# Performance work log

Hardware: AMD Instinct MI355X
Metric: run time of the kernel (lower is better)

Reference implementation:

```python
import jax, jax.numpy as jnp
import numpy as np

EMBED_DIM = 1024
N_HEADS = 16
HEAD_DIM = EMBED_DIM // N_HEADS
SEQ_LEN = 4096


def setup_inputs() -> dict:
    key = jax.random.key(0)
    k1, k2 = jax.random.split(key)
    x = jax.random.normal(k1, (SEQ_LEN, EMBED_DIM), dtype=jnp.float32)
    # Linear params (lecun-normal-ish scale)
    W_qkv = jax.random.normal(k2, (EMBED_DIM, 3 * EMBED_DIM), dtype=jnp.float32) / np.sqrt(EMBED_DIM)
    b_qkv = jnp.zeros((3 * EMBED_DIM,), dtype=jnp.float32)
    return {"x": x, "W_qkv": W_qkv, "b_qkv": b_qkv}


def reference(x, W_qkv, b_qkv):
    T = x.shape[0]
    # Fused QKV projection: [T, 3*E]
    qkv = x @ W_qkv + b_qkv
    q, k, v = jnp.split(qkv, 3, axis=-1)
    # [T, N, H]
    q = q.reshape(T, N_HEADS, HEAD_DIM)
    k = k.reshape(T, N_HEADS, HEAD_DIM)
    v = v.reshape(T, N_HEADS, HEAD_DIM)
    # Standard SDPA (module does NOT pass is_causal, so full attention)
    scale = 1.0 / np.sqrt(HEAD_DIM).astype(np.float32)
    logits = jnp.einsum("qnh,knh->nqk", q, k) * scale  # [N, T, T]
    attn = jax.nn.softmax(logits, axis=-1)
    y = jnp.einsum("nqk,knh->qnh", attn, v)  # [T, N, H]
    return y
```

## Files before the change

kernel.cpp:

```cpp
#include <hip/hip_runtime.h>

#define T_SEQ 4096
#define EMB   1024
#define NH    16
#define HD    64
#define N3    3072

#define SCL2 0.18033688011112042f

using u16 = unsigned short;
using u32 = unsigned int;
typedef __bf16 bf16x8 __attribute__((ext_vector_type(8)));
typedef float  f32x4  __attribute__((ext_vector_type(4)));
typedef float  f32x16 __attribute__((ext_vector_type(16)));
typedef u16    u16x4  __attribute__((ext_vector_type(4)));
typedef u16    u16x8  __attribute__((ext_vector_type(8)));

#if __has_builtin(__builtin_amdgcn_exp2f)
#define EXP2(x) __builtin_amdgcn_exp2f(x)
#else
#define EXP2(x) exp2f(x)
#endif

__device__ inline u16 f2bf(float f) {
    union { float f; unsigned u; } v; v.f = f;
    unsigned u = v.u;
    u += 0x7FFFu + ((u >> 16) & 1u);
    return (u16)(u >> 16);
}

__global__ void convert_x_kernel(const float* __restrict__ x, u16* __restrict__ xb) {
    int i = (blockIdx.x * 256 + threadIdx.x) * 8;
    float4 a = *(const float4*)(x + i);
    float4 b = *(const float4*)(x + i + 4);
    u16x8 o;
    o[0] = f2bf(a.x); o[1] = f2bf(a.y); o[2] = f2bf(a.z); o[3] = f2bf(a.w);
    o[4] = f2bf(b.x); o[5] = f2bf(b.y); o[6] = f2bf(b.z); o[7] = f2bf(b.w);
    *(u16x8*)(xb + i) = o;
}

__global__ void transpose_w_kernel(const float* __restrict__ W, u16* __restrict__ Wt) {
    __shared__ float tile[64][72];
    int n0 = blockIdx.x * 64, k0 = blockIdx.y * 64;
    float qs = (n0 < 1024) ? SCL2 : 1.0f;
    int t = threadIdx.x;
#pragma unroll
    for (int p = 0; p < 16; ++p) {
        int idx = p * 256 + t;
        int r = idx >> 6, c = idx & 63;
        tile[r][c] = W[(k0 + r) * N3 + n0 + c];
    }
    __syncthreads();
    int c2 = t >> 2;
    int kg = (t & 3) * 16;
    u16x8 o0, o1;
#pragma unroll
    for (int j = 0; j < 8; ++j) o0[j] = f2bf(tile[kg + j][c2] * qs);
#pragma unroll
    for (int j = 0; j < 8; ++j) o1[j] = f2bf(tile[kg + 8 + j][c2] * qs);
    u16* dst = Wt + (n0 + c2) * EMB + k0 + kg;
    *(u16x8*)dst = o0;
    *(u16x8*)(dst + 8) = o1;
}

__global__ __launch_bounds__(256) void gemm_qkv_kernel(const u16* __restrict__ xb,
                                                       const u16* __restrict__ Wt,
                                                       const float* __restrict__ bias,
                                                       u16* __restrict__ qkv,
                                                       u16* __restrict__ Vt) {
    __shared__ __align__(16) u16 Alds[2][128 * 64];
    __shared__ __align__(16) u16 Blds[2][128 * 64];
    int tid = threadIdx.x;
    int lane = tid & 63, wave = tid >> 6;
    int wm = wave >> 1, wn = wave & 1;
    int m0 = blockIdx.y * 128, n0 = blockIdx.x * 128;
    int lr = lane & 15, lg = lane >> 4;

    f32x4 acc[4][4] = {};

    int srow = tid >> 3;
    int cg = (tid & 7) << 3;
    int sg = (((tid & 7) ^ (srow & 7)) << 3);
    const u16* aBase = xb + (size_t)(m0 + srow) * EMB + cg;
    const u16* bBase = Wt + (size_t)(n0 + srow) * EMB + cg;
    int wIdx = srow * 64 + sg;

    u16x8 va[4], vb[4];
#pragma unroll
    for (int p = 0; p < 4; ++p) {
        va[p] = *(const u16x8*)(aBase + (size_t)(p * 32) * EMB);
        vb[p] = *(const u16x8*)(bBase + (size_t)(p * 32) * EMB);
    }

    for (int kt = 0; kt < 16; ++kt) {
        u16* Al = Alds[kt & 1];
        u16* Bl = Blds[kt & 1];
#pragma unroll
        for (int p = 0; p < 4; ++p) {
            *(u16x8*)&Al[wIdx + p * 32 * 64] = va[p];
            *(u16x8*)&Bl[wIdx + p * 32 * 64] = vb[p];
        }
        if (kt < 15) {
            int kbase = (kt + 1) * 64;
#pragma unroll
            for (int p = 0; p < 4; ++p) {
                va[p] = *(const u16x8*)(aBase + (size_t)(p * 32) * EMB + kbase);
                vb[p] = *(const u16x8*)(bBase + (size_t)(p * 32) * EMB + kbase);
            }
        }
        __syncthreads();
#pragma unroll
        for (int ks = 0; ks < 2; ++ks) {
            bf16x8 af[4], bf[4];
#pragma unroll
            for (int mi = 0; mi < 4; ++mi) {
                int row = wm * 64 + mi * 16 + lr;
                int rsg = ((ks * 4 + lg) ^ (row & 7)) << 3;
                af[mi] = *(const bf16x8*)&Al[row * 64 + rsg];
            }
#pragma unroll
            for (int ni = 0; ni < 4; ++ni) {
                int row = wn * 64 + ni * 16 + lr;
                int rsg = ((ks * 4 + lg) ^ (row & 7)) << 3;
                bf[ni] = *(const bf16x8*)&Bl[row * 64 + rsg];
            }
#pragma unroll
            for (int mi = 0; mi < 4; ++mi)
#pragma unroll
                for (int ni = 0; ni < 4; ++ni)
                    acc[mi][ni] = __builtin_amdgcn_mfma_f32_16x16x32_bf16(af[mi], bf[ni], acc[mi][ni], 0, 0, 0);
        }
    }
    if (n0 < 2048) {
#pragma unroll
        for (int ni = 0; ni < 4; ++ni) {
            int n = n0 + wn * 64 + ni * 16 + lr;
            float bv = bias[n];
            if (n < 1024) bv *= SCL2;
#pragma unroll
            for (int mi = 0; mi < 4; ++mi) {
                int mrow = m0 + wm * 64 + mi * 16 + lg * 4;
#pragma unroll
                for (int r = 0; r < 4; ++r)
                    qkv[(mrow + r) * N3 + n] = f2bf(acc[mi][ni][r] + bv);
            }
        }
    } else {
#pragma unroll
        for (int ni = 0; ni < 4; ++ni) {
            int n = n0 + wn * 64 + ni * 16 + lr;
            float bv = bias[n];
            int nc = n - 2048;
#pragma unroll
            for (int mi = 0; mi < 4; ++mi) {
                int mrow = m0 + wm * 64 + mi * 16 + lg * 4;
                u16x4 o;
#pragma unroll
                for (int r = 0; r < 4; ++r) o[r] = f2bf(acc[mi][ni][r] + bv);
                *(u16x4*)&Vt[(size_t)nc * T_SEQ + mrow] = o;
            }
        }
    }
}

__device__ inline u32 cvtpk(float lo, float hi) {
    u32 r;
    asm("v_cvt_pk_bf16_f32 %0, %1, %2" : "=v"(r) : "v"(lo), "v"(hi));
    return r;
}

__device__ inline bf16x8 mk8(u32 w0, u32 w1, u32 w2, u32 w3) {
    union { u32 w[4]; bf16x8 v; } u;
    u.w[0] = w0; u.w[1] = w1; u.w[2] = w2; u.w[3] = w3;
    return u.v;
}

__device__ inline void pack2(f32x16 p, int hi, bf16x8& fe, bf16x8& fo) {
    u32 a0 = cvtpk(p[0], p[1]),   a1 = cvtpk(p[2], p[3]);
    u32 a2 = cvtpk(p[4], p[5]),   a3 = cvtpk(p[6], p[7]);
    u32 b0 = cvtpk(p[8], p[9]),   b1 = cvtpk(p[10], p[11]);
    u32 b2 = cvtpk(p[12], p[13]), b3 = cvtpk(p[14], p[15]);
    u32 xa0 = (u32)__shfl_xor((int)a0, 32), xa1 = (u32)__shfl_xor((int)a1, 32);
    u32 xa2 = (u32)__shfl_xor((int)a2, 32), xa3 = (u32)__shfl_xor((int)a3, 32);
    u32 xb0 = (u32)__shfl_xor((int)b0, 32), xb1 = (u32)__shfl_xor((int)b1, 32);
    u32 xb2 = (u32)__shfl_xor((int)b2, 32), xb3 = (u32)__shfl_xor((int)b3, 32);
    fe = hi ? mk8(xa2, xa3, a2, a3) : mk8(a0, a1, xa0, xa1);
    fo = hi ? mk8(xb2, xb3, b2, b3) : mk8(b0, b1, xb0, xb1);
}

#define KVROW 72

__global__ __launch_bounds__(512, 2) void attn_kernel(const u16* __restrict__ qkv,
                                                      const u16* __restrict__ Vt,
                                                      float* __restrict__ out) {
    __shared__ __align__(16) char smem[69632];
    u16* K0 = (u16*)smem;
    u16* V0 = (u16*)(smem + 9216);
    u16* K1 = (u16*)(smem + 18432);
    u16* V1 = (u16*)(smem + 27648);

    int tid = threadIdx.x, lane = tid & 63, wave = tid >> 6;
    int ql = lane & 31, hi = lane >> 5;
    int bid = blockIdx.x;
    int idx = bid >> 3;
    int h = 2 * (bid & 7) + (idx >> 4);
    int q0 = (idx & 15) * 256;

    bf16x8 qf[4];
    {
        const u16* qp = qkv + (size_t)(q0 + wave * 32 + ql) * N3 + h * HD;
#pragma unroll
        for (int c = 0; c < 4; ++c)
            qf[c] = *(const bf16x8*)(qp + c * 16 + hi * 8);
    }

    bf16x8 ones;
    {
        union { u16x8 u; bf16x8 b; } uu;
#pragma unroll
        for (int j = 0; j < 8; ++j) uu.u[j] = 0x3F80;
        ones = uu.b;
    }

    f32x16 acc0 = {}, acc1 = {}, acc2 = {};

    int srow0 = tid >> 3, spg = tid & 7;
    const u16* kptr = qkv + EMB + h * HD;
    const u16* vptr = Vt + (size_t)(h * HD) * T_SEQ;
    int woff0 = srow0 * KVROW + spg * 8;

    u16x8 kst0 = *(const u16x8*)(kptr + (size_t)srow0 * N3 + spg * 8);
    u16x8 vst0 = *(const u16x8*)(vptr + (size_t)srow0 * T_SEQ + spg * 8);

    int koff = ql * KVROW + hi * 8;

    for (int t = 0; t < 64; ++t) {
        u16* Kl = (t & 1) ? K1 : K0;
        u16* Vl = (t & 1) ? V1 : V0;
        *(u16x8*)&Kl[woff0] = kst0;
        *(u16x8*)&Vl[woff0] = vst0;
        if (t < 63) {
            const u16* kb = kptr + (size_t)(t + 1) * 64 * N3;
            const u16* vb = vptr + (t + 1) * 64;
            kst0 = *(const u16x8*)(kb + (size_t)srow0 * N3 + spg * 8);
            vst0 = *(const u16x8*)(vb + (size_t)srow0 * T_SEQ + spg * 8);
        }
        __syncthreads();

        f32x16 s0 = {}, s1 = {};
#pragma unroll
        for (int c = 0; c < 4; ++c) {
            bf16x8 kf = *(const bf16x8*)&Kl[koff + c * 16];
            s0 = __builtin_amdgcn_mfma_f32_32x32x16_bf16(kf, qf[c], s0, 0, 0, 0);
        }
#pragma unroll
        for (int c = 0; c < 4; ++c) {
            bf16x8 kf = *(const bf16x8*)&Kl[koff + 32 * KVROW + c * 16];
            s1 = __builtin_amdgcn_mfma_f32_32x32x16_bf16(kf, qf[c], s1, 0, 0, 0);
        }

#pragma unroll
        for (int r = 0; r < 16; ++r) s0[r] = EXP2(s0[r]);
#pragma unroll
        for (int r = 0; r < 16; ++r) s1[r] = EXP2(s1[r]);

        bf16x8 pa0, pa1, pa2, pa3;
        pack2(s0, hi, pa0, pa1);
        pack2(s1, hi, pa2, pa3);

#pragma unroll
        for (int c = 0; c < 4; ++c) {
            bf16x8 pb = (c == 0) ? pa0 : (c == 1) ? pa1 : (c == 2) ? pa2 : pa3;
            bf16x8 vf0 = *(const bf16x8*)&Vl[koff + c * 16];
            acc0 = __builtin_amdgcn_mfma_f32_32x32x16_bf16(vf0, pb, acc0, 0, 0, 0);
            bf16x8 vf1 = *(const bf16x8*)&Vl[koff + 32 * KVROW + c * 16];
            acc1 = __builtin_amdgcn_mfma_f32_32x32x16_bf16(vf1, pb, acc1, 0, 0, 0);
            acc2 = __builtin_amdgcn_mfma_f32_32x32x16_bf16(ones, pb, acc2, 0, 0, 0);
        }
    }

    __syncthreads();

    float inv = 1.0f / acc2[0];
    float* ob = (float*)smem + wave * (32 * 68);
#pragma unroll
    for (int g = 0; g < 4; ++g) {
        f32x4 w0 = { acc0[4 * g] * inv, acc0[4 * g + 1] * inv, acc0[4 * g + 2] * inv, acc0[4 * g + 3] * inv };
        *(f32x4*)&ob[ql * 68 + 8 * g + 4 * hi] = w0;
        f32x4 w1 = { acc1[4 * g] * inv, acc1[4 * g + 1] * inv, acc1[4 * g + 2] * inv, acc1[4 * g + 3] * inv };
        *(f32x4*)&ob[ql * 68 + 32 + 8 * g + 4 * hi] = w1;
    }
    asm volatile("s_waitcnt lgkmcnt(0)" ::: "memory");
#pragma unroll
    for (int qq = 0; qq < 8; ++qq) {
        int q = qq * 4 + (lane >> 4);
        int d4 = (lane & 15) * 4;
        f32x4 v = *(const f32x4*)&ob[q * 68 + d4];
        *(f32x4*)&out[(size_t)(q0 + wave * 32 + q) * EMB + h * HD + d4] = v;
    }
}

extern "C" void kernel_launch(void* const* d_in, const int* in_sizes, int n_in,
                              void* d_out, int out_size, void* d_ws, size_t ws_size,
                              hipStream_t stream) {
    (void)in_sizes; (void)n_in; (void)out_size; (void)ws_size;
    const float* x = (const float*)d_in[0];
    const float* W = (const float*)d_in[1];
    const float* b = (const float*)d_in[2];
    float* out = (float*)d_out;

    u16* xb  = (u16*)d_ws;
    u16* Wt  = xb  + (size_t)T_SEQ * EMB;
    u16* qkv = Wt  + (size_t)N3 * EMB;
    u16* Vt  = qkv + (size_t)T_SEQ * N3;

    convert_x_kernel<<<(T_SEQ * EMB) / (256 * 8), 256, 0, stream>>>(x, xb);
    transpose_w_kernel<<<dim3(N3 / 64, EMB / 64), 256, 0, stream>>>(W, Wt);
    gemm_qkv_kernel<<<dim3(N3 / 128, T_SEQ / 128), 256, 0, stream>>>(xb, Wt, b, qkv, Vt);
    attn_kernel<<<256, 512, 0, stream>>>(qkv, Vt, out);
}
```

Before: 132.2 us.

## Split attention KV range across two blocks and add combine kernel

Each attention block now covers half of the key/value sequence, doubling the grid from 256 to 512 blocks so that more of the 256 CUs hold two resident blocks. Partial unnormalized outputs and row sums go to the output buffer and to scratch space that reuses the dead xb/Wt workspace. A new combine kernel adds the partials and normalizes them. Q and K are also written to separate contiguous buffers instead of the interleaved qkv layout. The cost is an extra kernel launch and extra fp32 global traffic for the partials. Skipping max-subtraction stays safe only because the two halves share the same implicit reference point.

```diff
diff --git a/kernel.cpp b/kernel.cpp
--- a/kernel.cpp
+++ b/kernel.cpp
@@ -66,7 +66,8 @@
 __global__ __launch_bounds__(256) void gemm_qkv_kernel(const u16* __restrict__ xb,
                                                        const u16* __restrict__ Wt,
                                                        const float* __restrict__ bias,
-                                                       u16* __restrict__ qkv,
+                                                       u16* __restrict__ Qp,
+                                                       u16* __restrict__ Kp,
                                                        u16* __restrict__ Vt) {
     __shared__ __align__(16) u16 Alds[2][128 * 64];
     __shared__ __align__(16) u16 Blds[2][128 * 64];
@@ -137,12 +138,14 @@
             int n = n0 + wn * 64 + ni * 16 + lr;
             float bv = bias[n];
             if (n < 1024) bv *= SCL2;
+            u16* pl = (n < 1024) ? Qp : Kp;
+            int nc = n & 1023;
 #pragma unroll
             for (int mi = 0; mi < 4; ++mi) {
                 int mrow = m0 + wm * 64 + mi * 16 + lg * 4;
 #pragma unroll
                 for (int r = 0; r < 4; ++r)
-                    qkv[(mrow + r) * N3 + n] = f2bf(acc[mi][ni][r] + bv);
+                    pl[(size_t)(mrow + r) * EMB + nc] = f2bf(acc[mi][ni][r] + bv);
             }
         }
     } else {
@@ -190,9 +193,14 @@
 
 #define KVROW 72
 
-__global__ __launch_bounds__(512, 2) void attn_kernel(const u16* __restrict__ qkv,
+__global__ __launch_bounds__(512, 2) void attn_kernel(const u16* __restrict__ Qp,
+                                                      const u16* __restrict__ Kp,
                                                       const u16* __restrict__ Vt,
-                                                      float* __restrict__ out) {
+                                                      float* __restrict__ out,
+                                                      float* __restrict__ pA,
+                                                      float* __restrict__ pB,
+                                                      float* __restrict__ l0,
+                                                      float* __restrict__ l1) {
     __shared__ __align__(16) char smem[69632];
     u16* K0 = (u16*)smem;
     u16* V0 = (u16*)(smem + 9216);
@@ -202,13 +210,15 @@
     int tid = threadIdx.x, lane = tid & 63, wave = tid >> 6;
     int ql = lane & 31, hi = lane >> 5;
     int bid = blockIdx.x;
-    int idx = bid >> 3;
-    int h = 2 * (bid & 7) + (idx >> 4);
+    int half = bid >> 8;
+    int rem = bid & 255;
+    int idx = rem >> 3;
+    int h = 2 * (rem & 7) + (idx >> 4);
     int q0 = (idx & 15) * 256;
 
     bf16x8 qf[4];
     {
-        const u16* qp = qkv + (size_t)(q0 + wave * 32 + ql) * N3 + h * HD;
+        const u16* qp = Qp + (size_t)(q0 + wave * 32 + ql) * EMB + h * HD;
 #pragma unroll
         for (int c = 0; c < 4; ++c)
             qf[c] = *(const bf16x8*)(qp + c * 16 + hi * 8);
@@ -225,24 +235,24 @@
     f32x16 acc0 = {}, acc1 = {}, acc2 = {};
 
     int srow0 = tid >> 3, spg = tid & 7;
-    const u16* kptr = qkv + EMB + h * HD;
-    const u16* vptr = Vt + (size_t)(h * HD) * T_SEQ;
+    const u16* kptr = Kp + (size_t)(half * 2048) * EMB + h * HD;
+    const u16* vptr = Vt + (size_t)(h * HD) * T_SEQ + half * 2048;
     int woff0 = srow0 * KVROW + spg * 8;
 
-    u16x8 kst0 = *(const u16x8*)(kptr + (size_t)srow0 * N3 + spg * 8);
+    u16x8 kst0 = *(const u16x8*)(kptr + (size_t)srow0 * EMB + spg * 8);
     u16x8 vst0 = *(const u16x8*)(vptr + (size_t)srow0 * T_SEQ + spg * 8);
 
     int koff = ql * KVROW + hi * 8;
 
-    for (int t = 0; t < 64; ++t) {
+    for (int t = 0; t < 32; ++t) {
         u16* Kl = (t & 1) ? K1 : K0;
         u16* Vl = (t & 1) ? V1 : V0;
         *(u16x8*)&Kl[woff0] = kst0;
         *(u16x8*)&Vl[woff0] = vst0;
-        if (t < 63) {
-            const u16* kb = kptr + (size_t)(t + 1) * 64 * N3;
+        if (t < 31) {
+            const u16* kb = kptr + (size_t)(t + 1) * 64 * EMB;
             const u16* vb = vptr + (t + 1) * 64;
-            kst0 = *(const u16x8*)(kb + (size_t)srow0 * N3 + spg * 8);
+            kst0 = *(const u16x8*)(kb + (size_t)srow0 * EMB + spg * 8);
             vst0 = *(const u16x8*)(vb + (size_t)srow0 * T_SEQ + spg * 8);
         }
         __syncthreads();
@@ -281,23 +291,58 @@
 
     __syncthreads();
 
-    float inv = 1.0f / acc2[0];
+    if (hi == 0) {
+        float* dl = half ? l1 : l0;
+        dl[h * T_SEQ + q0 + wave * 32 + ql] = acc2[0];
+    }
+
     float* ob = (float*)smem + wave * (32 * 68);
 #pragma unroll
     for (int g = 0; g < 4; ++g) {
-        f32x4 w0 = { acc0[4 * g] * inv, acc0[4 * g + 1] * inv, acc0[4 * g + 2] * inv, acc0[4 * g + 3] * inv };
+        f32x4 w0 = { acc0[4 * g], acc0[4 * g + 1], acc0[4 * g + 2], acc0[4 * g + 3] };
         *(f32x4*)&ob[ql * 68 + 8 * g + 4 * hi] = w0;
-        f32x4 w1 = { acc1[4 * g] * inv, acc1[4 * g + 1] * inv, acc1[4 * g + 2] * inv, acc1[4 * g + 3] * inv };
+        f32x4 w1 = { acc1[4 * g], acc1[4 * g + 1], acc1[4 * g + 2], acc1[4 * g + 3] };
         *(f32x4*)&ob[ql * 68 + 32 + 8 * g + 4 * hi] = w1;
     }
     asm volatile("s_waitcnt lgkmcnt(0)" ::: "memory");
-#pragma unroll
-    for (int qq = 0; qq < 8; ++qq) {
-        int q = qq * 4 + (lane >> 4);
-        int d4 = (lane & 15) * 4;
-        f32x4 v = *(const f32x4*)&ob[q * 68 + d4];
-        *(f32x4*)&out[(size_t)(q0 + wave * 32 + q) * EMB + h * HD + d4] = v;
-    }
+    if (half == 0) {
+#pragma unroll
+        for (int qq = 0; qq < 8; ++qq) {
+            int q = qq * 4 + (lane >> 4);
+            int d4 = (lane & 15) * 4;
+            f32x4 v = *(const f32x4*)&ob[q * 68 + d4];
+            *(f32x4*)&out[(size_t)(q0 + wave * 32 + q) * EMB + h * HD + d4] = v;
+        }
+    } else {
+        float* P1h = (h < 14) ? (pA + (size_t)h * (T_SEQ * HD))
+                              : (pB + (size_t)(h - 14) * (T_SEQ * HD));
+#pragma unroll
+        for (int qq = 0; qq < 8; ++qq) {
+            int q = qq * 4 + (lane >> 4);
+            int d4 = (lane & 15) * 4;
+            f32x4 v = *(const f32x4*)&ob[q * 68 + d4];
+            *(f32x4*)&P1h[(size_t)(q0 + wave * 32 + q) * HD + d4] = v;
+        }
+    }
+}
+
+__global__ void combine_kernel(float* __restrict__ out,
+                               const float* __restrict__ pA,
+                               const float* __restrict__ pB,
+                               const float* __restrict__ l0,
+                               const float* __restrict__ l1) {
+    size_t idx = ((size_t)blockIdx.x * 256 + threadIdx.x) * 4;
+    int q = (int)(idx >> 10);
+    int e = (int)(idx & 1023);
+    int h = e >> 6, d = e & 63;
+    const float* p1 = (h < 14) ? (pA + (size_t)h * (T_SEQ * HD))
+                               : (pB + (size_t)(h - 14) * (T_SEQ * HD));
+    f32x4 o = *(const f32x4*)&out[idx];
+    f32x4 p = *(const f32x4*)&p1[(size_t)q * HD + d];
+    float inv = 1.0f / (l0[h * T_SEQ + q] + l1[h * T_SEQ + q]);
+    f32x4 r = { (o[0] + p[0]) * inv, (o[1] + p[1]) * inv,
+                (o[2] + p[2]) * inv, (o[3] + p[3]) * inv };
+    *(f32x4*)&out[idx] = r;
 }
 
 extern "C" void kernel_launch(void* const* d_in, const int* in_sizes, int n_in,
@@ -309,13 +354,19 @@
     const float* b = (const float*)d_in[2];
     float* out = (float*)d_out;
 
-    u16* xb  = (u16*)d_ws;
-    u16* Wt  = xb  + (size_t)T_SEQ * EMB;
-    u16* qkv = Wt  + (size_t)N3 * EMB;
-    u16* Vt  = qkv + (size_t)T_SEQ * N3;
+    u16* xb = (u16*)d_ws;
+    u16* Wt = xb + (size_t)T_SEQ * EMB;
+    u16* Qp = Wt + (size_t)N3 * EMB;
+    u16* Kp = Qp + (size_t)T_SEQ * EMB;
+    u16* Vt = Kp + (size_t)T_SEQ * EMB;
+    float* pA = (float*)d_ws;
+    float* pB = (float*)(Vt + (size_t)EMB * T_SEQ);
+    float* l0 = pB + 2 * (size_t)T_SEQ * HD;
+    float* l1 = l0 + (size_t)NH * T_SEQ;
 
     convert_x_kernel<<<(T_SEQ * EMB) / (256 * 8), 256, 0, stream>>>(x, xb);
     transpose_w_kernel<<<dim3(N3 / 64, EMB / 64), 256, 0, stream>>>(W, Wt);
-    gemm_qkv_kernel<<<dim3(N3 / 128, T_SEQ / 128), 256, 0, stream>>>(xb, Wt, b, qkv, Vt);
-    attn_kernel<<<256, 512, 0, stream>>>(qkv, Vt, out);
-}
+    gemm_qkv_kernel<<<dim3(N3 / 128, T_SEQ / 128), 256, 0, stream>>>(xb, Wt, b, Qp, Kp, Vt);
+    attn_kernel<<<512, 512, 0, stream>>>(Qp, Kp, Vt, out, pA, pB, l0, l1);
+    combine_kernel<<<(T_SEQ * EMB) / (256 * 4), 256, 0, stream>>>(out, pA, pB, l0, l1);
+}
```

Measured after the change: 144.3 us. 9.1% more time.
